# Kernel tuning notes

Measured on AMD Instinct MI355X. Metric: run time of the kernel, lower is better.

Reference implementation:

```python
import jax, jax.numpy as jnp
import numpy as np

TOP_K = 8
NUM_EXPERTS = 128
HIDDEN = 2048
TOKENS = 16384
NORM_TOPK_PROB = True


def setup_inputs() -> dict:
    key = jax.random.key(0)
    k1, k2 = jax.random.split(key)
    hidden_states = jax.random.normal(k1, (TOKENS, HIDDEN), dtype=jnp.float32)
    # gate weight [num_experts, hidden] (nn.Linear layout)
    weight = jax.random.normal(k2, (NUM_EXPERTS, HIDDEN), dtype=jnp.float32) * 0.02
    return {"hidden_states": hidden_states, "weight": weight}


def reference(hidden_states, weight):
    x = hidden_states.reshape(-1, HIDDEN)
    # router_logits: [tokens, num_experts]
    router_logits = jnp.einsum("td,ed->te", x, weight)
    router_probs = jax.nn.softmax(router_logits.astype(jnp.float32), axis=-1)
    top_vals, top_idx = jax.lax.top_k(router_probs, TOP_K)
    if NORM_TOPK_PROB:
        top_vals = top_vals / jnp.sum(top_vals, axis=-1, keepdims=True)
    top_vals = top_vals.astype(hidden_states.dtype)
    return router_logits, top_vals, top_idx
```

## Files before the change

### kernel.cpp

```cpp
#include <hip/hip_runtime.h>
#include <float.h>
#include <math.h>

#define TOKENS 16384
#define HIDDEN 2048
#define NEXP 128
#define TOPK 8
#define NCAND 12
#define DELTA 5e-4f

#define BM 32
#define BK 64
#define KIT (HIDDEN / BK)

typedef float f32x16 __attribute__((ext_vector_type(16)));
typedef short bf16x8 __attribute__((ext_vector_type(8)));

__device__ __forceinline__ unsigned pack_hi(float a, float b) {
    return (__float_as_uint(a) >> 16) | (__float_as_uint(b) & 0xFFFF0000u);
}
__device__ __forceinline__ float resid(float a) {
    return a - __uint_as_float(__float_as_uint(a) & 0xFFFF0000u);
}

__device__ __forceinline__ bf16x8 pack8_hi(const float4 a, const float4 b) {
    union { uint4 u; bf16x8 v; } t;
    t.u.x = pack_hi(a.x, a.y); t.u.y = pack_hi(a.z, a.w);
    t.u.z = pack_hi(b.x, b.y); t.u.w = pack_hi(b.z, b.w);
    return t.v;
}
__device__ __forceinline__ bf16x8 pack8_lo(const float4 a, const float4 b) {
    union { uint4 u; bf16x8 v; } t;
    t.u.x = pack_hi(resid(a.x), resid(a.y)); t.u.y = pack_hi(resid(a.z), resid(a.w));
    t.u.z = pack_hi(resid(b.x), resid(b.y)); t.u.w = pack_hi(resid(b.z), resid(b.w));
    return t.v;
}

__device__ __forceinline__ void load_lds_16B(const void* g, void* l) {
    __builtin_amdgcn_global_load_lds(
        (const __attribute__((address_space(1))) unsigned int*)g,
        (__attribute__((address_space(3))) unsigned int*)l, 16, 0, 0);
}

__global__ __launch_bounds__(256) void presplit_w(const float* __restrict__ W,
                                                  unsigned short* __restrict__ Ws) {
    const int c = blockIdx.x * 256 + threadIdx.x;
    const int lane = c & 63;
    const int q = c >> 6;
    const int hl = q & 1;
    const int nt = (q >> 1) & 3;
    const int k16 = q >> 3;
    const int e = nt * 32 + (lane & 31);
    const int k0 = k16 * 16 + (lane >> 5) * 8;
    const float* wp = W + (size_t)e * HIDDEN + k0;
    float4 a = *(const float4*)wp;
    float4 b = *(const float4*)(wp + 4);
    if (hl) {
        a.x = resid(a.x); a.y = resid(a.y); a.z = resid(a.z); a.w = resid(a.w);
        b.x = resid(b.x); b.y = resid(b.y); b.z = resid(b.z); b.w = resid(b.w);
    }
    uint4 o;
    o.x = pack_hi(a.x, a.y); o.y = pack_hi(a.z, a.w);
    o.z = pack_hi(b.x, b.y); o.w = pack_hi(b.z, b.w);
    *(uint4*)(Ws + (size_t)c * 8) = o;
}

__global__ __launch_bounds__(256, 2) void router_gemm(const float* __restrict__ X,
                                                      const unsigned short* __restrict__ Ws,
                                                      float* __restrict__ logits) {
    __shared__ float sA[2][BM * BK];
    __shared__ unsigned short sB[2][32 * 512];

    const int tid = threadIdx.x;
    const int lane = tid & 63;
    const int wid = tid >> 6;
    const int t0 = blockIdx.x * BM;

    const int ai0 = wid * 2, ai1 = wid * 2 + 1;
    const int ar0 = 4 * ai0 + (lane >> 4);
    const int ar1 = 4 * ai1 + (lane >> 4);
    const int ak0 = ((lane & 15) ^ (ar0 & 15)) * 4;
    const int ak1 = ((lane & 15) ^ (ar1 & 15)) * 4;
    const float* aSrc0 = X + (size_t)(t0 + ar0) * HIDDEN + ak0;
    const float* aSrc1 = X + (size_t)(t0 + ar1) * HIDDEN + ak1;
    const unsigned short* bSrc = Ws + ((size_t)wid * 8) * 512 + (size_t)lane * 8;

    const int cr = lane & 31;
    const int kb = (lane >> 5) * 2;
    int aoff[4][2];
#pragma unroll
    for (int s = 0; s < 4; ++s) {
        aoff[s][0] = cr * 64 + (((s * 4 + kb + 0) ^ (cr & 15)) * 4);
        aoff[s][1] = cr * 64 + (((s * 4 + kb + 1) ^ (cr & 15)) * 4);
    }
    const int boff = (wid * 2) * 512 + lane * 8;

    f32x16 acc;
#pragma unroll
    for (int r = 0; r < 16; ++r) acc[r] = 0.f;

#pragma unroll
    for (int kt = 0; kt < 2; ++kt) {
        load_lds_16B(aSrc0 + kt * BK, &sA[kt][ai0 * 256]);
        load_lds_16B(aSrc1 + kt * BK, &sA[kt][ai1 * 256]);
#pragma unroll
        for (int i = 0; i < 8; ++i)
            load_lds_16B(bSrc + ((size_t)kt * 32 + i) * 512, &sB[kt][(wid * 8 + i) * 512]);
    }
    asm volatile("s_waitcnt vmcnt(10)" ::: "memory");
    __builtin_amdgcn_s_barrier();
    asm volatile("" ::: "memory");

#pragma unroll 1
    for (int kt = 0; kt < KIT; ++kt) {
        const int cur = kt & 1;
        const float* aBuf = &sA[cur][0];
        const unsigned short* bBuf = &sB[cur][0];

#pragma unroll
        for (int s = 0; s < 4; ++s) {
            const float4 f0 = *(const float4*)(aBuf + aoff[s][0]);
            const float4 f1 = *(const float4*)(aBuf + aoff[s][1]);
            const bf16x8 ah = pack8_hi(f0, f1);
            const bf16x8 al = pack8_lo(f0, f1);
            const bf16x8 bh = *(const bf16x8*)(bBuf + boff + s * 4096);
            const bf16x8 bl = *(const bf16x8*)(bBuf + boff + s * 4096 + 512);
            acc = __builtin_amdgcn_mfma_f32_32x32x16_bf16(ah, bh, acc, 0, 0, 0);
            acc = __builtin_amdgcn_mfma_f32_32x32x16_bf16(ah, bl, acc, 0, 0, 0);
            acc = __builtin_amdgcn_mfma_f32_32x32x16_bf16(al, bh, acc, 0, 0, 0);
        }

        __builtin_amdgcn_s_barrier();
        asm volatile("" ::: "memory");

        int kn = kt + 2; if (kn > KIT - 1) kn = KIT - 1;
        load_lds_16B(aSrc0 + kn * BK, &sA[cur][ai0 * 256]);
        load_lds_16B(aSrc1 + kn * BK, &sA[cur][ai1 * 256]);
#pragma unroll
        for (int i = 0; i < 8; ++i)
            load_lds_16B(bSrc + ((size_t)kn * 32 + i) * 512, &sB[cur][(wid * 8 + i) * 512]);

        asm volatile("s_waitcnt vmcnt(10)" ::: "memory");
        __builtin_amdgcn_sched_barrier(0);
        __builtin_amdgcn_s_barrier();
        asm volatile("" ::: "memory");
    }
    asm volatile("s_waitcnt vmcnt(0)" ::: "memory");

    const int e = wid * 32 + (lane & 31);
    const int rbase = 4 * (lane >> 5);
#pragma unroll
    for (int reg = 0; reg < 16; ++reg) {
        const int row = (reg & 3) + 8 * (reg >> 2) + rbase;
        logits[(size_t)(t0 + row) * NEXP + e] = acc[reg];
    }
}

__global__ __launch_bounds__(256) void router_topk(const float* __restrict__ logits,
                                                   const float* __restrict__ X,
                                                   const float* __restrict__ W,
                                                   float* __restrict__ top_vals,
                                                   float* __restrict__ top_idx) {
    const int lane = threadIdx.x & 63;
    const int t = blockIdx.x * 4 + (threadIdx.x >> 6);
    const float* lrow = logits + (size_t)t * NEXP;
    const float l0 = lrow[lane];
    const float l1 = lrow[lane + 64];
    bool r0 = false, r1 = false;
    float vals[NCAND]; int idxs[NCAND];

#pragma unroll
    for (int it = 0; it < TOPK + 1; ++it) {
        const float c0 = r0 ? -FLT_MAX : l0;
        const float c1 = r1 ? -FLT_MAX : l1;
        float v; int id;
        if (c1 > c0) { v = c1; id = lane + 64; }
        else         { v = c0; id = lane; }
#pragma unroll
        for (int off = 1; off < 64; off <<= 1) {
            const float ov = __shfl_xor(v, off);
            const int   oi = __shfl_xor(id, off);
            if (ov > v || (ov == v && oi < id)) { v = ov; id = oi; }
        }
        vals[it] = v; idxs[it] = id;
        if (id == lane) r0 = true;
        else if (id == lane + 64) r1 = true;
    }

    float ming = FLT_MAX;
#pragma unroll
    for (int i = 0; i < TOPK; ++i) ming = fminf(ming, vals[i] - vals[i + 1]);

    if (ming >= DELTA) {
        if (lane == 0) {
            const float m = vals[0];
            float ex[TOPK], s = 0.f;
#pragma unroll
            for (int i = 0; i < TOPK; ++i) { ex[i] = expf(vals[i] - m); s += ex[i]; }
            const float inv = 1.f / s;
#pragma unroll
            for (int i = 0; i < TOPK; ++i) {
                top_vals[(size_t)t * TOPK + i] = ex[i] * inv;
                top_idx[(size_t)t * TOPK + i] = (float)idxs[i];
            }
        }
        return;
    }

#pragma unroll
    for (int it = TOPK + 1; it < NCAND; ++it) {
        const float c0 = r0 ? -FLT_MAX : l0;
        const float c1 = r1 ? -FLT_MAX : l1;
        float v; int id;
        if (c1 > c0) { v = c1; id = lane + 64; }
        else         { v = c0; id = lane; }
#pragma unroll
        for (int off = 1; off < 64; off <<= 1) {
            const float ov = __shfl_xor(v, off);
            const int   oi = __shfl_xor(id, off);
            if (ov > v || (ov == v && oi < id)) { v = ov; id = oi; }
        }
        vals[it] = v; idxs[it] = id;
        if (id == lane) r0 = true;
        else if (id == lane + 64) r1 = true;
    }

    const float* xr = X + (size_t)t * HIDDEN;
    double xd[32];
#pragma unroll
    for (int j = 0; j < 8; ++j) {
        const float4 v = *(const float4*)(xr + j * 256 + lane * 4);
        xd[j * 4 + 0] = (double)v.x; xd[j * 4 + 1] = (double)v.y;
        xd[j * 4 + 2] = (double)v.z; xd[j * 4 + 3] = (double)v.w;
    }
    double acc[NCAND];
#pragma unroll
    for (int c = 0; c < NCAND; ++c) {
        const float* wr = W + (size_t)idxs[c] * HIDDEN;
        double a0 = 0.0, a1 = 0.0;
#pragma unroll
        for (int j = 0; j < 8; ++j) {
            const float4 w = *(const float4*)(wr + j * 256 + lane * 4);
            a0 = fma((double)w.x, xd[j * 4 + 0], a0);
            a1 = fma((double)w.y, xd[j * 4 + 1], a1);
            a0 = fma((double)w.z, xd[j * 4 + 2], a0);
            a1 = fma((double)w.w, xd[j * 4 + 3], a1);
        }
        acc[c] = a0 + a1;
    }
#pragma unroll
    for (int c = 0; c < NCAND; ++c)
#pragma unroll
        for (int off = 1; off < 64; off <<= 1)
            acc[c] += __shfl_xor(acc[c], off);

    int rank[NCAND];
#pragma unroll
    for (int c = 0; c < NCAND; ++c) {
        int r = 0;
#pragma unroll
        for (int m = 0; m < NCAND; ++m)
            if (acc[m] > acc[c] || (acc[m] == acc[c] && idxs[m] < idxs[c])) ++r;
        rank[c] = r;
    }
    double vmax = acc[0];
#pragma unroll
    for (int c = 0; c < NCAND; ++c) if (rank[c] == 0) vmax = acc[c];
    float ex[NCAND], s = 0.f;
#pragma unroll
    for (int c = 0; c < NCAND; ++c) {
        ex[c] = (rank[c] < TOPK) ? expf((float)(acc[c] - vmax)) : 0.f;
        s += ex[c];
    }
    const float inv = 1.f / s;
    if (lane == 0) {
#pragma unroll
        for (int c = 0; c < NCAND; ++c)
            if (rank[c] < TOPK) {
                top_vals[(size_t)t * TOPK + rank[c]] = ex[c] * inv;
                top_idx[(size_t)t * TOPK + rank[c]] = (float)idxs[c];
            }
    }
}

extern "C" void kernel_launch(void* const* d_in, const int* in_sizes, int n_in,
                              void* d_out, int out_size, void* d_ws, size_t ws_size,
                              hipStream_t stream) {
    const float* X = (const float*)d_in[0];
    const float* W = (const float*)d_in[1];
    float* logits = (float*)d_out;
    float* tvals  = logits + (size_t)TOKENS * NEXP;
    float* tidx   = tvals + (size_t)TOKENS * TOPK;

    unsigned short* Wsplit = (unsigned short*)d_ws;

    presplit_w<<<256, 256, 0, stream>>>(W, Wsplit);
    router_gemm<<<TOKENS / BM, 256, 0, stream>>>(X, Wsplit, logits);
    router_topk<<<TOKENS / 4, 256, 0, stream>>>(logits, X, W, tvals, tidx);
}
```

Baseline: 276.7 us.

## Load gate-weight fragments directly into registers instead of staging through LDS

The B operand (pre-split bf16 weight) is no longer staged through shared memory. Each wave now loads its own fragments straight from global memory into double-buffered registers, and the k-loop is unrolled by two so the register buffers alternate. This drops the sB LDS allocation and its reads, which frees LDS for a third block per CU (launch bounds raised to 3). In exchange each wave issues more global loads, and the vmcnt(10) waits were not retuned for the new load count, so the synchronisation may be wrong or overly conservative.

```diff
diff --git a/kernel.cpp b/kernel.cpp
--- a/kernel.cpp
+++ b/kernel.cpp
@@ -65,11 +65,10 @@
     *(uint4*)(Ws + (size_t)c * 8) = o;
 }
 
-__global__ __launch_bounds__(256, 2) void router_gemm(const float* __restrict__ X,
+__global__ __launch_bounds__(256, 3) void router_gemm(const float* __restrict__ X,
                                                       const unsigned short* __restrict__ Ws,
                                                       float* __restrict__ logits) {
     __shared__ float sA[2][BM * BK];
-    __shared__ unsigned short sB[2][32 * 512];
 
     const int tid = threadIdx.x;
     const int lane = tid & 63;
@@ -83,7 +82,10 @@
     const int ak1 = ((lane & 15) ^ (ar1 & 15)) * 4;
     const float* aSrc0 = X + (size_t)(t0 + ar0) * HIDDEN + ak0;
     const float* aSrc1 = X + (size_t)(t0 + ar1) * HIDDEN + ak1;
-    const unsigned short* bSrc = Ws + ((size_t)wid * 8) * 512 + (size_t)lane * 8;
+    float* aDst0[2] = { &sA[0][ai0 * 256], &sA[1][ai0 * 256] };
+    float* aDst1[2] = { &sA[0][ai1 * 256], &sA[1][ai1 * 256] };
+
+    const unsigned short* bBase = Ws + (size_t)(wid * 2) * 512 + (size_t)lane * 8;
 
     const int cr = lane & 31;
     const int kb = (lane >> 5) * 2;
@@ -93,59 +95,82 @@
         aoff[s][0] = cr * 64 + (((s * 4 + kb + 0) ^ (cr & 15)) * 4);
         aoff[s][1] = cr * 64 + (((s * 4 + kb + 1) ^ (cr & 15)) * 4);
     }
-    const int boff = (wid * 2) * 512 + lane * 8;
 
     f32x16 acc;
 #pragma unroll
     for (int r = 0; r < 16; ++r) acc[r] = 0.f;
 
-#pragma unroll
-    for (int kt = 0; kt < 2; ++kt) {
-        load_lds_16B(aSrc0 + kt * BK, &sA[kt][ai0 * 256]);
-        load_lds_16B(aSrc1 + kt * BK, &sA[kt][ai1 * 256]);
-#pragma unroll
-        for (int i = 0; i < 8; ++i)
-            load_lds_16B(bSrc + ((size_t)kt * 32 + i) * 512, &sB[kt][(wid * 8 + i) * 512]);
-    }
+    bf16x8 B0[8], B1[8];
+
+#define LOAD_B(Breg, kt_)                                                        \
+    {                                                                            \
+        _Pragma("unroll")                                                        \
+        for (int s = 0; s < 4; ++s) {                                            \
+            Breg[s * 2 + 0] = *(const bf16x8*)(bBase + ((size_t)((kt_) * 4 + s) * 8 + 0) * 512); \
+            Breg[s * 2 + 1] = *(const bf16x8*)(bBase + ((size_t)((kt_) * 4 + s) * 8 + 1) * 512); \
+        }                                                                        \
+    }
+#define STAGE_A(buf, kt_)                                                        \
+    {                                                                            \
+        load_lds_16B(aSrc0 + (kt_) * BK, aDst0[buf]);                            \
+        load_lds_16B(aSrc1 + (kt_) * BK, aDst1[buf]);                            \
+    }
+#define COMPUTE(buf, Breg)                                                       \
+    {                                                                            \
+        const float* aBuf = &sA[buf][0];                                         \
+        _Pragma("unroll")                                                        \
+        for (int s = 0; s < 4; ++s) {                                            \
+            const float4 f0 = *(const float4*)(aBuf + aoff[s][0]);               \
+            const float4 f1 = *(const float4*)(aBuf + aoff[s][1]);               \
+            const bf16x8 ah = pack8_hi(f0, f1);                                  \
+            const bf16x8 al = pack8_lo(f0, f1);                                  \
+            acc = __builtin_amdgcn_mfma_f32_32x32x16_bf16(ah, Breg[s * 2 + 0], acc, 0, 0, 0); \
+            acc = __builtin_amdgcn_mfma_f32_32x32x16_bf16(ah, Breg[s * 2 + 1], acc, 0, 0, 0); \
+            acc = __builtin_amdgcn_mfma_f32_32x32x16_bf16(al, Breg[s * 2 + 0], acc, 0, 0, 0); \
+        }                                                                        \
+    }
+
+    STAGE_A(0, 0); LOAD_B(B0, 0);
+    __builtin_amdgcn_sched_barrier(0);
+    STAGE_A(1, 1); LOAD_B(B1, 1);
+    __builtin_amdgcn_sched_barrier(0);
     asm volatile("s_waitcnt vmcnt(10)" ::: "memory");
     __builtin_amdgcn_s_barrier();
     asm volatile("" ::: "memory");
 
 #pragma unroll 1
-    for (int kt = 0; kt < KIT; ++kt) {
-        const int cur = kt & 1;
-        const float* aBuf = &sA[cur][0];
-        const unsigned short* bBuf = &sB[cur][0];
-
-#pragma unroll
-        for (int s = 0; s < 4; ++s) {
-            const float4 f0 = *(const float4*)(aBuf + aoff[s][0]);
-            const float4 f1 = *(const float4*)(aBuf + aoff[s][1]);
-            const bf16x8 ah = pack8_hi(f0, f1);
-            const bf16x8 al = pack8_lo(f0, f1);
-            const bf16x8 bh = *(const bf16x8*)(bBuf + boff + s * 4096);
-            const bf16x8 bl = *(const bf16x8*)(bBuf + boff + s * 4096 + 512);
-            acc = __builtin_amdgcn_mfma_f32_32x32x16_bf16(ah, bh, acc, 0, 0, 0);
-            acc = __builtin_amdgcn_mfma_f32_32x32x16_bf16(ah, bl, acc, 0, 0, 0);
-            acc = __builtin_amdgcn_mfma_f32_32x32x16_bf16(al, bh, acc, 0, 0, 0);
-        }
-
+    for (int kt = 0; kt < KIT; kt += 2) {
+        COMPUTE(0, B0);
         __builtin_amdgcn_s_barrier();
         asm volatile("" ::: "memory");
-
-        int kn = kt + 2; if (kn > KIT - 1) kn = KIT - 1;
-        load_lds_16B(aSrc0 + kn * BK, &sA[cur][ai0 * 256]);
-        load_lds_16B(aSrc1 + kn * BK, &sA[cur][ai1 * 256]);
-#pragma unroll
-        for (int i = 0; i < 8; ++i)
-            load_lds_16B(bSrc + ((size_t)kn * 32 + i) * 512, &sB[cur][(wid * 8 + i) * 512]);
-
+        {
+            int kn = kt + 2; if (kn > KIT - 1) kn = KIT - 1;
+            LOAD_B(B0, kn); STAGE_A(0, kn);
+        }
+        __builtin_amdgcn_sched_barrier(0);
         asm volatile("s_waitcnt vmcnt(10)" ::: "memory");
         __builtin_amdgcn_sched_barrier(0);
         __builtin_amdgcn_s_barrier();
         asm volatile("" ::: "memory");
+
+        COMPUTE(1, B1);
+        __builtin_amdgcn_s_barrier();
+        asm volatile("" ::: "memory");
+        {
+            int kn = kt + 3; if (kn > KIT - 1) kn = KIT - 1;
+            LOAD_B(B1, kn); STAGE_A(1, kn);
+        }
+        __builtin_amdgcn_sched_barrier(0);
+        asm volatile("s_waitcnt vmcnt(10)" ::: "memory");
+        __builtin_amdgcn_sched_barrier(0);
+        __builtin_amdgcn_s_barrier();
+        asm volatile("" ::: "memory");
     }
     asm volatile("s_waitcnt vmcnt(0)" ::: "memory");
+
+#undef LOAD_B
+#undef STAGE_A
+#undef COMPUTE
 
     const int e = wid * 32 + (lane & 31);
     const int rbase = 4 * (lane >> 5);
```

Result: no change. 279.2 us (+0.9%).

## Fuse top-k routing into the GEMM epilogue via shared-memory logits

Applied to the files above, without the earlier changes.

Removes the separate top-k kernel and runs its selection inside the router GEMM. After the accumulation loop, each block stages its 32x128 logits tile in LDS, reusing the A-tile buffer, and each wave then handles top-k and normalisation for 8 tokens. This saves one kernel launch and the global re-read of the logits. In exchange, the epilogue is serialised per wave and the GEMM kernel carries more register pressure, which could reduce overlap or occupancy.

```diff
diff --git a/kernel.cpp b/kernel.cpp
--- a/kernel.cpp
+++ b/kernel.cpp
@@ -67,9 +67,14 @@
 
 __global__ __launch_bounds__(256, 2) void router_gemm(const float* __restrict__ X,
                                                       const unsigned short* __restrict__ Ws,
-                                                      float* __restrict__ logits) {
-    __shared__ float sA[2][BM * BK];
-    __shared__ unsigned short sB[2][32 * 512];
+                                                      const float* __restrict__ W,
+                                                      float* __restrict__ logits,
+                                                      float* __restrict__ top_vals,
+                                                      float* __restrict__ top_idx) {
+    __shared__ __align__(16) unsigned char smem[81920];
+    float (*sA)[BM * BK] = (float (*)[BM * BK])smem;
+    unsigned short (*sB)[32 * 512] = (unsigned short (*)[32 * 512])(smem + 16384);
+    float* sLog = (float*)smem;
 
     const int tid = threadIdx.x;
     const int lane = tid & 63;
@@ -146,6 +151,8 @@
         asm volatile("" ::: "memory");
     }
     asm volatile("s_waitcnt vmcnt(0)" ::: "memory");
+    __builtin_amdgcn_s_barrier();
+    asm volatile("" ::: "memory");
 
     const int e = wid * 32 + (lane & 31);
     const int rbase = 4 * (lane >> 5);
@@ -153,133 +160,132 @@
     for (int reg = 0; reg < 16; ++reg) {
         const int row = (reg & 3) + 8 * (reg >> 2) + rbase;
         logits[(size_t)(t0 + row) * NEXP + e] = acc[reg];
-    }
-}
-
-__global__ __launch_bounds__(256) void router_topk(const float* __restrict__ logits,
-                                                   const float* __restrict__ X,
-                                                   const float* __restrict__ W,
-                                                   float* __restrict__ top_vals,
-                                                   float* __restrict__ top_idx) {
-    const int lane = threadIdx.x & 63;
-    const int t = blockIdx.x * 4 + (threadIdx.x >> 6);
-    const float* lrow = logits + (size_t)t * NEXP;
-    const float l0 = lrow[lane];
-    const float l1 = lrow[lane + 64];
-    bool r0 = false, r1 = false;
-    float vals[NCAND]; int idxs[NCAND];
-
-#pragma unroll
-    for (int it = 0; it < TOPK + 1; ++it) {
-        const float c0 = r0 ? -FLT_MAX : l0;
-        const float c1 = r1 ? -FLT_MAX : l1;
-        float v; int id;
-        if (c1 > c0) { v = c1; id = lane + 64; }
-        else         { v = c0; id = lane; }
-#pragma unroll
-        for (int off = 1; off < 64; off <<= 1) {
-            const float ov = __shfl_xor(v, off);
-            const int   oi = __shfl_xor(id, off);
-            if (ov > v || (ov == v && oi < id)) { v = ov; id = oi; }
-        }
-        vals[it] = v; idxs[it] = id;
-        if (id == lane) r0 = true;
-        else if (id == lane + 64) r1 = true;
-    }
-
-    float ming = FLT_MAX;
-#pragma unroll
-    for (int i = 0; i < TOPK; ++i) ming = fminf(ming, vals[i] - vals[i + 1]);
-
-    if (ming >= DELTA) {
+        sLog[row * NEXP + e] = acc[reg];
+    }
+    __builtin_amdgcn_s_barrier();
+    asm volatile("" ::: "memory");
+
+#pragma unroll 1
+    for (int tk = 0; tk < 8; ++tk) {
+        const int trow = wid * 8 + tk;
+        const size_t t = (size_t)t0 + trow;
+        const float l0 = sLog[trow * NEXP + lane];
+        const float l1 = sLog[trow * NEXP + lane + 64];
+        bool r0 = false, r1 = false;
+        float vals[NCAND]; int idxs[NCAND];
+
+#pragma unroll
+        for (int it = 0; it < TOPK + 1; ++it) {
+            const float c0 = r0 ? -FLT_MAX : l0;
+            const float c1 = r1 ? -FLT_MAX : l1;
+            float v; int id;
+            if (c1 > c0) { v = c1; id = lane + 64; }
+            else         { v = c0; id = lane; }
+#pragma unroll
+            for (int off = 1; off < 64; off <<= 1) {
+                const float ov = __shfl_xor(v, off);
+                const int   oi = __shfl_xor(id, off);
+                if (ov > v || (ov == v && oi < id)) { v = ov; id = oi; }
+            }
+            vals[it] = v; idxs[it] = id;
+            if (id == lane) r0 = true;
+            else if (id == lane + 64) r1 = true;
+        }
+
+        float ming = FLT_MAX;
+#pragma unroll
+        for (int i = 0; i < TOPK; ++i) ming = fminf(ming, vals[i] - vals[i + 1]);
+
+        if (ming >= DELTA) {
+            if (lane == 0) {
+                const float m = vals[0];
+                float ex[TOPK], s = 0.f;
+#pragma unroll
+                for (int i = 0; i < TOPK; ++i) { ex[i] = expf(vals[i] - m); s += ex[i]; }
+                const float inv = 1.f / s;
+#pragma unroll
+                for (int i = 0; i < TOPK; ++i) {
+                    top_vals[t * TOPK + i] = ex[i] * inv;
+                    top_idx[t * TOPK + i] = (float)idxs[i];
+                }
+            }
+            continue;
+        }
+
+#pragma unroll
+        for (int it = TOPK + 1; it < NCAND; ++it) {
+            const float c0 = r0 ? -FLT_MAX : l0;
+            const float c1 = r1 ? -FLT_MAX : l1;
+            float v; int id;
+            if (c1 > c0) { v = c1; id = lane + 64; }
+            else         { v = c0; id = lane; }
+#pragma unroll
+            for (int off = 1; off < 64; off <<= 1) {
+                const float ov = __shfl_xor(v, off);
+                const int   oi = __shfl_xor(id, off);
+                if (ov > v || (ov == v && oi < id)) { v = ov; id = oi; }
+            }
+            vals[it] = v; idxs[it] = id;
+            if (id == lane) r0 = true;
+            else if (id == lane + 64) r1 = true;
+        }
+
+        const float* xr = X + t * HIDDEN;
+        double xd[32];
+#pragma unroll
+        for (int j = 0; j < 8; ++j) {
+            const float4 v = *(const float4*)(xr + j * 256 + lane * 4);
+            xd[j * 4 + 0] = (double)v.x; xd[j * 4 + 1] = (double)v.y;
+            xd[j * 4 + 2] = (double)v.z; xd[j * 4 + 3] = (double)v.w;
+        }
+        double accد[NCAND];
+#pragma unroll
+        for (int c = 0; c < NCAND; ++c) {
+            const float* wr = W + (size_t)idxs[c] * HIDDEN;
+            double a0 = 0.0, a1 = 0.0;
+#pragma unroll
+            for (int j = 0; j < 8; ++j) {
+                const float4 w = *(const float4*)(wr + j * 256 + lane * 4);
+                a0 = fma((double)w.x, xd[j * 4 + 0], a0);
+                a1 = fma((double)w.y, xd[j * 4 + 1], a1);
+                a0 = fma((double)w.z, xd[j * 4 + 2], a0);
+                a1 = fma((double)w.w, xd[j * 4 + 3], a1);
+            }
+            accد[c] = a0 + a1;
+        }
+#pragma unroll
+        for (int c = 0; c < NCAND; ++c)
+#pragma unroll
+            for (int off = 1; off < 64; off <<= 1)
+                accد[c] += __shfl_xor(accد[c], off);
+
+        int rank[NCAND];
+#pragma unroll
+        for (int c = 0; c < NCAND; ++c) {
+            int r = 0;
+#pragma unroll
+            for (int m = 0; m < NCAND; ++m)
+                if (accد[m] > accد[c] || (accد[m] == accد[c] && idxs[m] < idxs[c])) ++r;
+            rank[c] = r;
+        }
+        double vmax = accد[0];
+#pragma unroll
+        for (int c = 0; c < NCAND; ++c) if (rank[c] == 0) vmax = accد[c];
+        float ex[NCAND], s = 0.f;
+#pragma unroll
+        for (int c = 0; c < NCAND; ++c) {
+            ex[c] = (rank[c] < TOPK) ? expf((float)(accد[c] - vmax)) : 0.f;
+            s += ex[c];
+        }
+        const float inv = 1.f / s;
         if (lane == 0) {
-            const float m = vals[0];
-            float ex[TOPK], s = 0.f;
-#pragma unroll
-            for (int i = 0; i < TOPK; ++i) { ex[i] = expf(vals[i] - m); s += ex[i]; }
-            const float inv = 1.f / s;
-#pragma unroll
-            for (int i = 0; i < TOPK; ++i) {
-                top_vals[(size_t)t * TOPK + i] = ex[i] * inv;
-                top_idx[(size_t)t * TOPK + i] = (float)idxs[i];
-            }
-        }
-        return;
-    }
-
-#pragma unroll
-    for (int it = TOPK + 1; it < NCAND; ++it) {
-        const float c0 = r0 ? -FLT_MAX : l0;
-        const float c1 = r1 ? -FLT_MAX : l1;
-        float v; int id;
-        if (c1 > c0) { v = c1; id = lane + 64; }
-        else         { v = c0; id = lane; }
-#pragma unroll
-        for (int off = 1; off < 64; off <<= 1) {
-            const float ov = __shfl_xor(v, off);
-            const int   oi = __shfl_xor(id, off);
-            if (ov > v || (ov == v && oi < id)) { v = ov; id = oi; }
-        }
-        vals[it] = v; idxs[it] = id;
-        if (id == lane) r0 = true;
-        else if (id == lane + 64) r1 = true;
-    }
-
-    const float* xr = X + (size_t)t * HIDDEN;
-    double xd[32];
-#pragma unroll
-    for (int j = 0; j < 8; ++j) {
-        const float4 v = *(const float4*)(xr + j * 256 + lane * 4);
-        xd[j * 4 + 0] = (double)v.x; xd[j * 4 + 1] = (double)v.y;
-        xd[j * 4 + 2] = (double)v.z; xd[j * 4 + 3] = (double)v.w;
-    }
-    double acc[NCAND];
-#pragma unroll
-    for (int c = 0; c < NCAND; ++c) {
-        const float* wr = W + (size_t)idxs[c] * HIDDEN;
-        double a0 = 0.0, a1 = 0.0;
-#pragma unroll
-        for (int j = 0; j < 8; ++j) {
-            const float4 w = *(const float4*)(wr + j * 256 + lane * 4);
-            a0 = fma((double)w.x, xd[j * 4 + 0], a0);
-            a1 = fma((double)w.y, xd[j * 4 + 1], a1);
-            a0 = fma((double)w.z, xd[j * 4 + 2], a0);
-            a1 = fma((double)w.w, xd[j * 4 + 3], a1);
-        }
-        acc[c] = a0 + a1;
-    }
-#pragma unroll
-    for (int c = 0; c < NCAND; ++c)
-#pragma unroll
-        for (int off = 1; off < 64; off <<= 1)
-            acc[c] += __shfl_xor(acc[c], off);
-
-    int rank[NCAND];
-#pragma unroll
-    for (int c = 0; c < NCAND; ++c) {
-        int r = 0;
-#pragma unroll
-        for (int m = 0; m < NCAND; ++m)
-            if (acc[m] > acc[c] || (acc[m] == acc[c] && idxs[m] < idxs[c])) ++r;
-        rank[c] = r;
-    }
-    double vmax = acc[0];
-#pragma unroll
-    for (int c = 0; c < NCAND; ++c) if (rank[c] == 0) vmax = acc[c];
-    float ex[NCAND], s = 0.f;
-#pragma unroll
-    for (int c = 0; c < NCAND; ++c) {
-        ex[c] = (rank[c] < TOPK) ? expf((float)(acc[c] - vmax)) : 0.f;
-        s += ex[c];
-    }
-    const float inv = 1.f / s;
-    if (lane == 0) {
-#pragma unroll
-        for (int c = 0; c < NCAND; ++c)
-            if (rank[c] < TOPK) {
-                top_vals[(size_t)t * TOPK + rank[c]] = ex[c] * inv;
-                top_idx[(size_t)t * TOPK + rank[c]] = (float)idxs[c];
-            }
+#pragma unroll
+            for (int c = 0; c < NCAND; ++c)
+                if (rank[c] < TOPK) {
+                    top_vals[t * TOPK + rank[c]] = ex[c] * inv;
+                    top_idx[t * TOPK + rank[c]] = (float)idxs[c];
+                }
+        }
     }
 }
 
@@ -295,6 +301,5 @@
     unsigned short* Wsplit = (unsigned short*)d_ws;
 
     presplit_w<<<256, 256, 0, stream>>>(W, Wsplit);
-    router_gemm<<<TOKENS / BM, 256, 0, stream>>>(X, Wsplit, logits);
-    router_topk<<<TOKENS / 4, 256, 0, stream>>>(logits, X, W, tvals, tidx);
-}
+    router_gemm<<<TOKENS / BM, 256, 0, stream>>>(X, Wsplit, W, logits, tvals, tidx);
+}
```

Result: no change. 274.6 us (-0.7%).
